# Kernel optimization log

Hardware: AMD Instinct MI355X
Metric: run time of the kernel (lower is better)

Reference implementation:

```python
import jax, jax.numpy as jnp
import numpy as np

B, S, IN_DIM, OUT_DIM, DV = 64, 8192, 512, 128, 128


def setup_inputs() -> dict:
    key = jax.random.key(0)
    k1, k2, k3, k4, k5 = jax.random.split(key, 5)
    # xavier_uniform bound = sqrt(6/(fan_in+fan_out))
    bk = float(np.sqrt(6.0 / (OUT_DIM + OUT_DIM)))
    bq = float(np.sqrt(6.0 / (IN_DIM + OUT_DIM)))
    return {
        "k": jax.random.normal(k1, (B, S, OUT_DIM), dtype=jnp.float32),
        "q": jax.random.normal(k2, (B, IN_DIM), dtype=jnp.float32),
        "v": jax.random.normal(k3, (B, S, DV), dtype=jnp.float32),
        "Wk": jax.random.uniform(k4, (OUT_DIM, OUT_DIM), jnp.float32, -bk, bk),
        "Wq": jax.random.uniform(k5, (IN_DIM, OUT_DIM), jnp.float32, -bq, bq),
    }


def reference(k, q, v, Wk, Wq):
    scale = jnp.sqrt(jnp.asarray(OUT_DIM, dtype=k.dtype))
    key = jnp.einsum("bsd,de->bse", k, Wk)          # [B,S,out_dim]
    query = q @ Wq                                     # [B,out_dim]
    score = jnp.einsum("be,bse->bs", query, key) / scale  # [B,S]
    attn = jax.nn.softmax(score, axis=-1)              # [B,S]
    context = jnp.einsum("bs,bsv->bv", attn, v)       # [B,dv]
    return context
```

## Files before the change

### kernel.cpp

```cpp
#include <hip/hip_runtime.h>
#include <math.h>

#define BB 64
#define SS 8192
#define IN_DIM 512
#define OUT_DIM 128
#define DVV 128
#define CHUNK 256
#define NCHUNK (SS / CHUNK)

__global__ void qt_kernel(const float* __restrict__ q,
                          const float* __restrict__ Wq,
                          const float* __restrict__ Wk,
                          float* __restrict__ qt) {
    int b = blockIdx.x;
    int e = threadIdx.x;
    __shared__ float qs[OUT_DIM];
    const float* qb = q + (size_t)b * IN_DIM;
    float acc = 0.f;
    for (int i = 0; i < IN_DIM; ++i)
        acc = fmaf(qb[i], Wq[(size_t)i * OUT_DIM + e], acc);
    qs[e] = acc;
    __syncthreads();
    float a2 = 0.f;
    const float* wkrow = Wk + (size_t)e * OUT_DIM;
    for (int i = 0; i < OUT_DIM; ++i)
        a2 = fmaf(wkrow[i], qs[i], a2);
    qt[(size_t)b * OUT_DIM + e] = a2 * 0.08838834764831845f;
}

__global__ __launch_bounds__(256) void partial_kernel(
    const float* __restrict__ k, const float* __restrict__ v,
    const float* __restrict__ qt, float* __restrict__ ml,
    float* __restrict__ ctx) {
    int blk = blockIdx.x;
    int b = blk / NCHUNK;
    int c = blk % NCHUNK;
    int s0 = c * CHUNK;
    int t = threadIdx.x;
    int wave = t >> 6, lane = t & 63, half = lane >> 5, l32 = lane & 31;

    __shared__ float4 qts4[OUT_DIM / 4];
    __shared__ float sc[CHUNK];
    __shared__ float4 red[256];
    __shared__ float wred[4];

    if (t < OUT_DIM / 4)
        qts4[t] = ((const float4*)(qt + (size_t)b * OUT_DIM))[t];
    __syncthreads();

    const float4* k4 = (const float4*)(k + (size_t)b * SS * OUT_DIM);
    float4 qv = qts4[l32];
    for (int i = wave * 2 + half; i < CHUNK; i += 8) {
        float4 kv = k4[(size_t)(s0 + i) * (OUT_DIM / 4) + l32];
        float p = kv.x * qv.x + kv.y * qv.y + kv.z * qv.z + kv.w * qv.w;
        p += __shfl_xor(p, 1);
        p += __shfl_xor(p, 2);
        p += __shfl_xor(p, 4);
        p += __shfl_xor(p, 8);
        p += __shfl_xor(p, 16);
        if (l32 == 0) sc[i] = p;
    }
    __syncthreads();

    float m = -INFINITY;
    for (int i = t; i < CHUNK; i += 256) m = fmaxf(m, sc[i]);
    for (int d = 1; d < 64; d <<= 1) m = fmaxf(m, __shfl_xor(m, d));
    if (lane == 0) wred[wave] = m;
    __syncthreads();
    m = fmaxf(fmaxf(wred[0], wred[1]), fmaxf(wred[2], wred[3]));
    __syncthreads();

    float lsum = 0.f;
    for (int i = t; i < CHUNK; i += 256) {
        float e = __expf(sc[i] - m);
        sc[i] = e;
        lsum += e;
    }
    for (int d = 1; d < 64; d <<= 1) lsum += __shfl_xor(lsum, d);
    if (lane == 0) wred[wave] = lsum;
    __syncthreads();
    lsum = wred[0] + wred[1] + wred[2] + wred[3];

    int col = t & 31;
    int rg = t >> 5;
    const float4* v4 = (const float4*)(v + (size_t)b * SS * DVV);
    float4 acc = make_float4(0.f, 0.f, 0.f, 0.f);
    for (int i = rg; i < CHUNK; i += 8) {
        float p = sc[i];
        float4 vv = v4[(size_t)(s0 + i) * (DVV / 4) + col];
        acc.x = fmaf(p, vv.x, acc.x);
        acc.y = fmaf(p, vv.y, acc.y);
        acc.z = fmaf(p, vv.z, acc.z);
        acc.w = fmaf(p, vv.w, acc.w);
    }
    red[t] = acc;
    __syncthreads();
    for (int off = 128; off >= 32; off >>= 1) {
        if (t < off) {
            float4 o = red[t + off];
            red[t].x += o.x; red[t].y += o.y;
            red[t].z += o.z; red[t].w += o.w;
        }
        __syncthreads();
    }
    if (t < 32)
        ((float4*)(ctx + ((size_t)(b * NCHUNK + c)) * DVV))[t] = red[t];
    if (t == 0) {
        ml[(b * NCHUNK + c) * 2 + 0] = m;
        ml[(b * NCHUNK + c) * 2 + 1] = lsum;
    }
}

__global__ void combine_kernel(const float* __restrict__ ml,
                               const float* __restrict__ ctx,
                               float* __restrict__ out) {
    int b = blockIdx.x;
    int t = threadIdx.x;
    __shared__ float ms, ls;
    float m = -INFINITY;
    if (t < NCHUNK) m = ml[(b * NCHUNK + t) * 2];
    for (int d = 1; d < 32; d <<= 1) m = fmaxf(m, __shfl_xor(m, d));
    if (t == 0) ms = m;
    __syncthreads();
    m = ms;
    float l = 0.f;
    if (t < NCHUNK)
        l = ml[(b * NCHUNK + t) * 2 + 1] * __expf(ml[(b * NCHUNK + t) * 2] - m);
    for (int d = 1; d < 32; d <<= 1) l += __shfl_xor(l, d);
    if (t == 0) ls = l;
    __syncthreads();
    l = ls;
    float acc = 0.f;
    for (int c2 = 0; c2 < NCHUNK; ++c2) {
        float w = __expf(ml[(b * NCHUNK + c2) * 2] - m);
        acc = fmaf(ctx[((size_t)(b * NCHUNK + c2)) * DVV + t], w, acc);
    }
    out[(size_t)b * DVV + t] = acc / l;
}

extern "C" void kernel_launch(void* const* d_in, const int* in_sizes, int n_in,
                              void* d_out, int out_size, void* d_ws, size_t ws_size,
                              hipStream_t stream) {
    const float* k  = (const float*)d_in[0];
    const float* q  = (const float*)d_in[1];
    const float* v  = (const float*)d_in[2];
    const float* Wk = (const float*)d_in[3];
    const float* Wq = (const float*)d_in[4];
    float* out = (float*)d_out;

    float* qt  = (float*)d_ws;
    float* ml  = qt + BB * OUT_DIM;
    float* ctx = ml + BB * NCHUNK * 2;

    qt_kernel<<<BB, OUT_DIM, 0, stream>>>(q, Wq, Wk, qt);
    partial_kernel<<<BB * NCHUNK, 256, 0, stream>>>(k, v, qt, ml, ctx);
    combine_kernel<<<BB, DVV, 0, stream>>>(ml, ctx, out);
}
```

Measured before the change: 119.5 us.

## Fuse score, softmax and V accumulation into single-pass online softmax per chunk

The partial kernel now streams K and V rows together. Each 32-lane group keeps a running max, sum and context accumulator using online softmax rescaling, and the groups are merged once through shared memory. This replaces the separate score pass, the max and sum reductions and the second V pass, along with their barriers, so K and V loads can overlap. The qt kernel also splits its two matvec reductions across 512 threads. The cost is two extra exponentials per row per lane.

```diff
diff --git a/kernel.cpp b/kernel.cpp
--- a/kernel.cpp
+++ b/kernel.cpp
@@ -9,24 +9,35 @@
 #define CHUNK 256
 #define NCHUNK (SS / CHUNK)
 
-__global__ void qt_kernel(const float* __restrict__ q,
+__global__ __launch_bounds__(512) void qt_kernel(const float* __restrict__ q,
                           const float* __restrict__ Wq,
                           const float* __restrict__ Wk,
                           float* __restrict__ qt) {
     int b = blockIdx.x;
-    int e = threadIdx.x;
+    int t = threadIdx.x;
+    int e = t & 127;
+    int h = t >> 7;
+    __shared__ float part[4][OUT_DIM];
     __shared__ float qs[OUT_DIM];
+
     const float* qb = q + (size_t)b * IN_DIM;
     float acc = 0.f;
-    for (int i = 0; i < IN_DIM; ++i)
+    for (int i = h * (IN_DIM / 4); i < (h + 1) * (IN_DIM / 4); ++i)
         acc = fmaf(qb[i], Wq[(size_t)i * OUT_DIM + e], acc);
-    qs[e] = acc;
+    part[h][e] = acc;
     __syncthreads();
+    if (h == 0) qs[e] = part[0][e] + part[1][e] + part[2][e] + part[3][e];
+    __syncthreads();
+
     float a2 = 0.f;
     const float* wkrow = Wk + (size_t)e * OUT_DIM;
-    for (int i = 0; i < OUT_DIM; ++i)
+    for (int i = h * (OUT_DIM / 4); i < (h + 1) * (OUT_DIM / 4); ++i)
         a2 = fmaf(wkrow[i], qs[i], a2);
-    qt[(size_t)b * OUT_DIM + e] = a2 * 0.08838834764831845f;
+    part[h][e] = a2;
+    __syncthreads();
+    if (h == 0)
+        qt[(size_t)b * OUT_DIM + e] =
+            (part[0][e] + part[1][e] + part[2][e] + part[3][e]) * 0.08838834764831845f;
 }
 
 __global__ __launch_bounds__(256) void partial_kernel(
@@ -38,77 +49,74 @@
     int c = blk % NCHUNK;
     int s0 = c * CHUNK;
     int t = threadIdx.x;
-    int wave = t >> 6, lane = t & 63, half = lane >> 5, l32 = lane & 31;
+    int g = t >> 5;
+    int l32 = t & 31;
 
     __shared__ float4 qts4[OUT_DIM / 4];
-    __shared__ float sc[CHUNK];
-    __shared__ float4 red[256];
-    __shared__ float wred[4];
+    __shared__ float gm[8], gl[8];
+    __shared__ float4 gacc[8][32];
 
     if (t < OUT_DIM / 4)
         qts4[t] = ((const float4*)(qt + (size_t)b * OUT_DIM))[t];
     __syncthreads();
+    float4 qv = qts4[l32];
 
     const float4* k4 = (const float4*)(k + (size_t)b * SS * OUT_DIM);
-    float4 qv = qts4[l32];
-    for (int i = wave * 2 + half; i < CHUNK; i += 8) {
-        float4 kv = k4[(size_t)(s0 + i) * (OUT_DIM / 4) + l32];
+    const float4* v4 = (const float4*)(v + (size_t)b * SS * DVV);
+
+    float m = -INFINITY, l = 0.f;
+    float4 acc = make_float4(0.f, 0.f, 0.f, 0.f);
+
+    #pragma unroll 4
+    for (int j = 0; j < CHUNK / 8; ++j) {
+        int i = s0 + g + 8 * j;
+        float4 kv = k4[(size_t)i * (OUT_DIM / 4) + l32];
+        float4 vv = v4[(size_t)i * (DVV / 4) + l32];
         float p = kv.x * qv.x + kv.y * qv.y + kv.z * qv.z + kv.w * qv.w;
         p += __shfl_xor(p, 1);
         p += __shfl_xor(p, 2);
         p += __shfl_xor(p, 4);
         p += __shfl_xor(p, 8);
         p += __shfl_xor(p, 16);
-        if (l32 == 0) sc[i] = p;
+        float mnew = fmaxf(m, p);
+        float cr = __expf(m - mnew);
+        float e = __expf(p - mnew);
+        l = l * cr + e;
+        acc.x = fmaf(acc.x, cr, e * vv.x);
+        acc.y = fmaf(acc.y, cr, e * vv.y);
+        acc.z = fmaf(acc.z, cr, e * vv.z);
+        acc.w = fmaf(acc.w, cr, e * vv.w);
+        m = mnew;
     }
+
+    if (l32 == 0) gm[g] = m;
+    __syncthreads();
+    float M = gm[0];
+    #pragma unroll
+    for (int i = 1; i < 8; ++i) M = fmaxf(M, gm[i]);
+    float scale = __expf(m - M);
+    if (l32 == 0) gl[g] = l * scale;
+    float4 sa;
+    sa.x = acc.x * scale; sa.y = acc.y * scale;
+    sa.z = acc.z * scale; sa.w = acc.w * scale;
+    gacc[g][l32] = sa;
     __syncthreads();
 
-    float m = -INFINITY;
-    for (int i = t; i < CHUNK; i += 256) m = fmaxf(m, sc[i]);
-    for (int d = 1; d < 64; d <<= 1) m = fmaxf(m, __shfl_xor(m, d));
-    if (lane == 0) wred[wave] = m;
-    __syncthreads();
-    m = fmaxf(fmaxf(wred[0], wred[1]), fmaxf(wred[2], wred[3]));
-    __syncthreads();
-
-    float lsum = 0.f;
-    for (int i = t; i < CHUNK; i += 256) {
-        float e = __expf(sc[i] - m);
-        sc[i] = e;
-        lsum += e;
+    if (t < 32) {
+        float4 r = gacc[0][t];
+        #pragma unroll
+        for (int i2 = 1; i2 < 8; ++i2) {
+            float4 o = gacc[i2][t];
+            r.x += o.x; r.y += o.y; r.z += o.z; r.w += o.w;
+        }
+        ((float4*)(ctx + ((size_t)(b * NCHUNK + c)) * DVV))[t] = r;
     }
-    for (int d = 1; d < 64; d <<= 1) lsum += __shfl_xor(lsum, d);
-    if (lane == 0) wred[wave] = lsum;
-    __syncthreads();
-    lsum = wred[0] + wred[1] + wred[2] + wred[3];
-
-    int col = t & 31;
-    int rg = t >> 5;
-    const float4* v4 = (const float4*)(v + (size_t)b * SS * DVV);
-    float4 acc = make_float4(0.f, 0.f, 0.f, 0.f);
-    for (int i = rg; i < CHUNK; i += 8) {
-        float p = sc[i];
-        float4 vv = v4[(size_t)(s0 + i) * (DVV / 4) + col];
-        acc.x = fmaf(p, vv.x, acc.x);
-        acc.y = fmaf(p, vv.y, acc.y);
-        acc.z = fmaf(p, vv.z, acc.z);
-        acc.w = fmaf(p, vv.w, acc.w);
-    }
-    red[t] = acc;
-    __syncthreads();
-    for (int off = 128; off >= 32; off >>= 1) {
-        if (t < off) {
-            float4 o = red[t + off];
-            red[t].x += o.x; red[t].y += o.y;
-            red[t].z += o.z; red[t].w += o.w;
-        }
-        __syncthreads();
-    }
-    if (t < 32)
-        ((float4*)(ctx + ((size_t)(b * NCHUNK + c)) * DVV))[t] = red[t];
     if (t == 0) {
-        ml[(b * NCHUNK + c) * 2 + 0] = m;
-        ml[(b * NCHUNK + c) * 2 + 1] = lsum;
+        float L = gl[0];
+        #pragma unroll
+        for (int i3 = 1; i3 < 8; ++i3) L += gl[i3];
+        ml[(b * NCHUNK + c) * 2 + 0] = M;
+        ml[(b * NCHUNK + c) * 2 + 1] = L;
     }
 }
 
@@ -153,7 +161,7 @@
     float* ml  = qt + BB * OUT_DIM;
     float* ctx = ml + BB * NCHUNK * 2;
 
-    qt_kernel<<<BB, OUT_DIM, 0, stream>>>(q, Wq, Wk, qt);
+    qt_kernel<<<BB, 512, 0, stream>>>(q, Wq, Wk, qt);
     partial_kernel<<<BB * NCHUNK, 256, 0, stream>>>(k, v, qt, ml, ctx);
     combine_kernel<<<BB, DVV, 0, stream>>>(ml, ctx, out);
 }
```

Measured after the change: 147.4 us. 1.23x slower.

## Split partial kernel into score and context kernels with global-normalized weights

Applied to the files above, without the earlier changes.

Splits the fused per-chunk kernel into a score kernel, which writes raw scores and per-chunk max/sum, and a context kernel. The context kernel recomputes the global max and normalizer and applies final softmax weights before the V reduction, so the combine step becomes a plain sum. It also parallelizes the query-transform kernel over 4x more threads and fully unrolls the K and V loops. The cost is an extra launch and a round trip of the scores through global memory, and the K and V streams no longer share one kernel.

```diff
diff --git a/kernel.cpp b/kernel.cpp
--- a/kernel.cpp
+++ b/kernel.cpp
@@ -9,49 +9,61 @@
 #define CHUNK 256
 #define NCHUNK (SS / CHUNK)
 
-__global__ void qt_kernel(const float* __restrict__ q,
+__global__ __launch_bounds__(512) void qt_kernel(const float* __restrict__ q,
                           const float* __restrict__ Wq,
                           const float* __restrict__ Wk,
                           float* __restrict__ qt) {
     int b = blockIdx.x;
-    int e = threadIdx.x;
+    int t = threadIdx.x;
+    int e = t & 127;
+    int h = t >> 7;
+    __shared__ float part[4][OUT_DIM];
     __shared__ float qs[OUT_DIM];
+
     const float* qb = q + (size_t)b * IN_DIM;
     float acc = 0.f;
-    for (int i = 0; i < IN_DIM; ++i)
+    for (int i = h * (IN_DIM / 4); i < (h + 1) * (IN_DIM / 4); ++i)
         acc = fmaf(qb[i], Wq[(size_t)i * OUT_DIM + e], acc);
-    qs[e] = acc;
+    part[h][e] = acc;
     __syncthreads();
+    if (h == 0) qs[e] = part[0][e] + part[1][e] + part[2][e] + part[3][e];
+    __syncthreads();
+
     float a2 = 0.f;
     const float* wkrow = Wk + (size_t)e * OUT_DIM;
-    for (int i = 0; i < OUT_DIM; ++i)
+    for (int i = h * (OUT_DIM / 4); i < (h + 1) * (OUT_DIM / 4); ++i)
         a2 = fmaf(wkrow[i], qs[i], a2);
-    qt[(size_t)b * OUT_DIM + e] = a2 * 0.08838834764831845f;
+    part[h][e] = a2;
+    __syncthreads();
+    if (h == 0)
+        qt[(size_t)b * OUT_DIM + e] =
+            (part[0][e] + part[1][e] + part[2][e] + part[3][e]) * 0.08838834764831845f;
 }
 
-__global__ __launch_bounds__(256) void partial_kernel(
-    const float* __restrict__ k, const float* __restrict__ v,
-    const float* __restrict__ qt, float* __restrict__ ml,
-    float* __restrict__ ctx) {
+__global__ __launch_bounds__(256) void score_kernel(
+    const float* __restrict__ k, const float* __restrict__ qt,
+    float* __restrict__ scores, float* __restrict__ ml) {
     int blk = blockIdx.x;
-    int b = blk / NCHUNK;
-    int c = blk % NCHUNK;
+    int b = blk >> 5;
+    int c = blk & 31;
     int s0 = c * CHUNK;
     int t = threadIdx.x;
     int wave = t >> 6, lane = t & 63, half = lane >> 5, l32 = lane & 31;
 
     __shared__ float4 qts4[OUT_DIM / 4];
     __shared__ float sc[CHUNK];
-    __shared__ float4 red[256];
     __shared__ float wred[4];
 
     if (t < OUT_DIM / 4)
         qts4[t] = ((const float4*)(qt + (size_t)b * OUT_DIM))[t];
     __syncthreads();
+    float4 qv = qts4[l32];
 
     const float4* k4 = (const float4*)(k + (size_t)b * SS * OUT_DIM);
-    float4 qv = qts4[l32];
-    for (int i = wave * 2 + half; i < CHUNK; i += 8) {
+    int r = wave * 2 + half;
+    #pragma unroll
+    for (int j = 0; j < CHUNK / 8; ++j) {
+        int i = r + 8 * j;
         float4 kv = k4[(size_t)(s0 + i) * (OUT_DIM / 4) + l32];
         float p = kv.x * qv.x + kv.y * qv.y + kv.z * qv.z + kv.w * qv.w;
         p += __shfl_xor(p, 1);
@@ -63,36 +75,64 @@
     }
     __syncthreads();
 
-    float m = -INFINITY;
-    for (int i = t; i < CHUNK; i += 256) m = fmaxf(m, sc[i]);
+    float s = sc[t];
+    scores[(size_t)b * SS + s0 + t] = s;
+
+    float m = s;
     for (int d = 1; d < 64; d <<= 1) m = fmaxf(m, __shfl_xor(m, d));
     if (lane == 0) wred[wave] = m;
     __syncthreads();
     m = fmaxf(fmaxf(wred[0], wred[1]), fmaxf(wred[2], wred[3]));
     __syncthreads();
 
-    float lsum = 0.f;
-    for (int i = t; i < CHUNK; i += 256) {
-        float e = __expf(sc[i] - m);
-        sc[i] = e;
-        lsum += e;
+    float l = __expf(s - m);
+    for (int d = 1; d < 64; d <<= 1) l += __shfl_xor(l, d);
+    if (lane == 0) wred[wave] = l;
+    __syncthreads();
+    if (t == 0) {
+        ml[blk * 2 + 0] = m;
+        ml[blk * 2 + 1] = wred[0] + wred[1] + wred[2] + wred[3];
     }
-    for (int d = 1; d < 64; d <<= 1) lsum += __shfl_xor(lsum, d);
-    if (lane == 0) wred[wave] = lsum;
+}
+
+__global__ __launch_bounds__(256) void ctx_kernel(
+    const float* __restrict__ v, const float* __restrict__ scores,
+    const float* __restrict__ ml, float* __restrict__ ctx) {
+    int blk = blockIdx.x;
+    int b = blk >> 5;
+    int c = blk & 31;
+    int s0 = c * CHUNK;
+    int t = threadIdx.x;
+
+    __shared__ float mlsh[NCHUNK * 2];
+    __shared__ float wl[CHUNK];
+    __shared__ float4 red[256];
+
+    if (t < NCHUNK * 2) mlsh[t] = ml[b * NCHUNK * 2 + t];
     __syncthreads();
-    lsum = wred[0] + wred[1] + wred[2] + wred[3];
+    float M = mlsh[0];
+    #pragma unroll
+    for (int i = 1; i < NCHUNK; ++i) M = fmaxf(M, mlsh[2 * i]);
+    float L = 0.f;
+    #pragma unroll
+    for (int i = 0; i < NCHUNK; ++i) L += mlsh[2 * i + 1] * __expf(mlsh[2 * i] - M);
+    float invL = 1.f / L;
 
-    int col = t & 31;
-    int rg = t >> 5;
+    wl[t] = __expf(scores[(size_t)b * SS + s0 + t] - M) * invL;
+    __syncthreads();
+
+    int col = t & 31, rg = t >> 5;
     const float4* v4 = (const float4*)(v + (size_t)b * SS * DVV);
     float4 acc = make_float4(0.f, 0.f, 0.f, 0.f);
-    for (int i = rg; i < CHUNK; i += 8) {
-        float p = sc[i];
+    #pragma unroll
+    for (int j = 0; j < CHUNK / 8; ++j) {
+        int i = rg + 8 * j;
         float4 vv = v4[(size_t)(s0 + i) * (DVV / 4) + col];
-        acc.x = fmaf(p, vv.x, acc.x);
-        acc.y = fmaf(p, vv.y, acc.y);
-        acc.z = fmaf(p, vv.z, acc.z);
-        acc.w = fmaf(p, vv.w, acc.w);
+        float w = wl[i];
+        acc.x = fmaf(w, vv.x, acc.x);
+        acc.y = fmaf(w, vv.y, acc.y);
+        acc.z = fmaf(w, vv.z, acc.z);
+        acc.w = fmaf(w, vv.w, acc.w);
     }
     red[t] = acc;
     __syncthreads();
@@ -105,38 +145,17 @@
         __syncthreads();
     }
     if (t < 32)
-        ((float4*)(ctx + ((size_t)(b * NCHUNK + c)) * DVV))[t] = red[t];
-    if (t == 0) {
-        ml[(b * NCHUNK + c) * 2 + 0] = m;
-        ml[(b * NCHUNK + c) * 2 + 1] = lsum;
-    }
+        ((float4*)(ctx + (size_t)blk * DVV))[t] = red[t];
 }
 
-__global__ void combine_kernel(const float* __restrict__ ml,
-                               const float* __restrict__ ctx,
-                               float* __restrict__ out) {
+__global__ void sum_kernel(const float* __restrict__ ctx, float* __restrict__ out) {
     int b = blockIdx.x;
     int t = threadIdx.x;
-    __shared__ float ms, ls;
-    float m = -INFINITY;
-    if (t < NCHUNK) m = ml[(b * NCHUNK + t) * 2];
-    for (int d = 1; d < 32; d <<= 1) m = fmaxf(m, __shfl_xor(m, d));
-    if (t == 0) ms = m;
-    __syncthreads();
-    m = ms;
-    float l = 0.f;
-    if (t < NCHUNK)
-        l = ml[(b * NCHUNK + t) * 2 + 1] * __expf(ml[(b * NCHUNK + t) * 2] - m);
-    for (int d = 1; d < 32; d <<= 1) l += __shfl_xor(l, d);
-    if (t == 0) ls = l;
-    __syncthreads();
-    l = ls;
     float acc = 0.f;
-    for (int c2 = 0; c2 < NCHUNK; ++c2) {
-        float w = __expf(ml[(b * NCHUNK + c2) * 2] - m);
-        acc = fmaf(ctx[((size_t)(b * NCHUNK + c2)) * DVV + t], w, acc);
-    }
-    out[(size_t)b * DVV + t] = acc / l;
+    #pragma unroll
+    for (int c = 0; c < NCHUNK; ++c)
+        acc += ctx[((size_t)b * NCHUNK + c) * DVV + t];
+    out[(size_t)b * DVV + t] = acc;
 }
 
 extern "C" void kernel_launch(void* const* d_in, const int* in_sizes, int n_in,
@@ -149,11 +168,13 @@
     const float* Wq = (const float*)d_in[4];
     float* out = (float*)d_out;
 
-    float* qt  = (float*)d_ws;
-    float* ml  = qt + BB * OUT_DIM;
-    float* ctx = ml + BB * NCHUNK * 2;
+    float* qt     = (float*)d_ws;
+    float* ml     = qt + BB * OUT_DIM;
+    float* ctx    = ml + BB * NCHUNK * 2;
+    float* scores = ctx + BB * NCHUNK * DVV;
 
-    qt_kernel<<<BB, OUT_DIM, 0, stream>>>(q, Wq, Wk, qt);
-    partial_kernel<<<BB * NCHUNK, 256, 0, stream>>>(k, v, qt, ml, ctx);
-    combine_kernel<<<BB, DVV, 0, stream>>>(ml, ctx, out);
+    qt_kernel<<<BB, 512, 0, stream>>>(q, Wq, Wk, qt);
+    score_kernel<<<BB * NCHUNK, 256, 0, stream>>>(k, qt, scores, ml);
+    ctx_kernel<<<BB * NCHUNK, 256, 0, stream>>>(v, scores, ml, ctx);
+    sum_kernel<<<BB, DVV, 0, stream>>>(ctx, out);
 }
```

Result: slower. 149.8 us (+25.4%).

## Halve chunk size, split qt reduction across 512 threads, rework combine

Applied to the files above, without the earlier changes.

Halves the sequence chunk per block, which doubles the number of partial blocks to 4096 so more blocks are in flight while streaming K and V. qt_kernel now splits both matvec reductions across four thread groups and sums the parts in shared memory, cutting its serial dependency chain. combine_kernel loads the 128 (m, l) pairs per batch into shared memory and has every thread compute the global max and sum itself. This replaces the old 32-lane shuffle reductions, which covered only 32 chunks and would be wrong with 64. The cost is twice as many partial results written and then read back in combine, plus more per-block setup overhead.

```diff
diff --git a/kernel.cpp b/kernel.cpp
--- a/kernel.cpp
+++ b/kernel.cpp
@@ -6,27 +6,38 @@
 #define IN_DIM 512
 #define OUT_DIM 128
 #define DVV 128
-#define CHUNK 256
+#define CHUNK 128
 #define NCHUNK (SS / CHUNK)
 
-__global__ void qt_kernel(const float* __restrict__ q,
+__global__ __launch_bounds__(512) void qt_kernel(const float* __restrict__ q,
                           const float* __restrict__ Wq,
                           const float* __restrict__ Wk,
                           float* __restrict__ qt) {
     int b = blockIdx.x;
-    int e = threadIdx.x;
+    int t = threadIdx.x;
+    int e = t & 127;
+    int h = t >> 7;
+    __shared__ float part[4][OUT_DIM];
     __shared__ float qs[OUT_DIM];
+
     const float* qb = q + (size_t)b * IN_DIM;
     float acc = 0.f;
-    for (int i = 0; i < IN_DIM; ++i)
+    for (int i = h * (IN_DIM / 4); i < (h + 1) * (IN_DIM / 4); ++i)
         acc = fmaf(qb[i], Wq[(size_t)i * OUT_DIM + e], acc);
-    qs[e] = acc;
+    part[h][e] = acc;
     __syncthreads();
+    if (h == 0) qs[e] = part[0][e] + part[1][e] + part[2][e] + part[3][e];
+    __syncthreads();
+
     float a2 = 0.f;
     const float* wkrow = Wk + (size_t)e * OUT_DIM;
-    for (int i = 0; i < OUT_DIM; ++i)
+    for (int i = h * (OUT_DIM / 4); i < (h + 1) * (OUT_DIM / 4); ++i)
         a2 = fmaf(wkrow[i], qs[i], a2);
-    qt[(size_t)b * OUT_DIM + e] = a2 * 0.08838834764831845f;
+    part[h][e] = a2;
+    __syncthreads();
+    if (h == 0)
+        qt[(size_t)b * OUT_DIM + e] =
+            (part[0][e] + part[1][e] + part[2][e] + part[3][e]) * 0.08838834764831845f;
 }
 
 __global__ __launch_bounds__(256) void partial_kernel(
@@ -34,8 +45,8 @@
     const float* __restrict__ qt, float* __restrict__ ml,
     float* __restrict__ ctx) {
     int blk = blockIdx.x;
-    int b = blk / NCHUNK;
-    int c = blk % NCHUNK;
+    int b = blk >> 6;
+    int c = blk & 63;
     int s0 = c * CHUNK;
     int t = threadIdx.x;
     int wave = t >> 6, lane = t & 63, half = lane >> 5, l32 = lane & 31;
@@ -105,38 +116,36 @@
         __syncthreads();
     }
     if (t < 32)
-        ((float4*)(ctx + ((size_t)(b * NCHUNK + c)) * DVV))[t] = red[t];
+        ((float4*)(ctx + (size_t)blk * DVV))[t] = red[t];
     if (t == 0) {
-        ml[(b * NCHUNK + c) * 2 + 0] = m;
-        ml[(b * NCHUNK + c) * 2 + 1] = lsum;
+        ml[blk * 2 + 0] = m;
+        ml[blk * 2 + 1] = lsum;
     }
 }
 
-__global__ void combine_kernel(const float* __restrict__ ml,
-                               const float* __restrict__ ctx,
-                               float* __restrict__ out) {
+__global__ __launch_bounds__(128) void combine_kernel(
+    const float* __restrict__ ml, const float* __restrict__ ctx,
+    float* __restrict__ out) {
     int b = blockIdx.x;
     int t = threadIdx.x;
-    __shared__ float ms, ls;
-    float m = -INFINITY;
-    if (t < NCHUNK) m = ml[(b * NCHUNK + t) * 2];
-    for (int d = 1; d < 32; d <<= 1) m = fmaxf(m, __shfl_xor(m, d));
-    if (t == 0) ms = m;
+    __shared__ float mls[NCHUNK * 2];
+
+    mls[t] = ml[b * NCHUNK * 2 + t];
     __syncthreads();
-    m = ms;
-    float l = 0.f;
-    if (t < NCHUNK)
-        l = ml[(b * NCHUNK + t) * 2 + 1] * __expf(ml[(b * NCHUNK + t) * 2] - m);
-    for (int d = 1; d < 32; d <<= 1) l += __shfl_xor(l, d);
-    if (t == 0) ls = l;
-    __syncthreads();
-    l = ls;
+
+    float M = -INFINITY;
+    #pragma unroll 8
+    for (int c = 0; c < NCHUNK; ++c) M = fmaxf(M, mls[2 * c]);
+    float L = 0.f;
+    #pragma unroll 8
+    for (int c = 0; c < NCHUNK; ++c) L += mls[2 * c + 1] * __expf(mls[2 * c] - M);
+
     float acc = 0.f;
-    for (int c2 = 0; c2 < NCHUNK; ++c2) {
-        float w = __expf(ml[(b * NCHUNK + c2) * 2] - m);
-        acc = fmaf(ctx[((size_t)(b * NCHUNK + c2)) * DVV + t], w, acc);
-    }
-    out[(size_t)b * DVV + t] = acc / l;
+    const float* cb = ctx + (size_t)b * NCHUNK * DVV + t;
+    #pragma unroll 8
+    for (int c = 0; c < NCHUNK; ++c)
+        acc = fmaf(cb[(size_t)c * DVV], __expf(mls[2 * c] - M), acc);
+    out[(size_t)b * DVV + t] = acc / L;
 }
 
 extern "C" void kernel_launch(void* const* d_in, const int* in_sizes, int n_in,
@@ -151,9 +160,9 @@
 
     float* qt  = (float*)d_ws;
     float* ml  = qt + BB * OUT_DIM;
-    float* ctx = ml + BB * NCHUNK * 2;
+    float* ctx = ml + (size_t)BB * NCHUNK * 2;
 
-    qt_kernel<<<BB, OUT_DIM, 0, stream>>>(q, Wq, Wk, qt);
+    qt_kernel<<<BB, 512, 0, stream>>>(q, Wq, Wk, qt);
     partial_kernel<<<BB * NCHUNK, 256, 0, stream>>>(k, v, qt, ml, ctx);
-    combine_kernel<<<BB, DVV, 0, stream>>>(ml, ctx, out);
+    combine_kernel<<<BB, 128, 0, stream>>>(ml, ctx, out);
 }
```

New measurement: 151.5 us. +26.9%, slower.
